# Optimization experiments

Measured on AMD Instinct MI355X. Metric: run time of the kernel, lower is better.

Reference implementation:

```python
import jax, jax.numpy as jnp
import numpy as np

THRESHOLD_FACTOR = 1.25

def setup_inputs() -> dict:
    key = jax.random.key(0)
    r_embed = jax.random.normal(key, (2, 4096, 2), dtype=jnp.float32)
    return {"r_embed": r_embed}

def reference(r_embed):
    # r_embed: [b, n, 2]
    # diff[b,s,t,i] = -r[b,s,i]*r[b,t,i] + r[b,s,i]   (einsum('bsi,bti->bsti', r, -r) + r.unsqueeze(2))
    diff = -r_embed[:, :, None, :] * r_embed[:, None, :, :] + r_embed[:, :, None, :]  # [b,s,t,2]
    dist_sq = jnp.sum(diff * diff, axis=-1)                                            # [b,s,t]
    phase_diff = jnp.arctan2(diff[..., 1], diff[..., 0])
    forward_bias = 0.5 * (1.0 + jnp.cos(phase_diff)) * jnp.exp(-dist_sq)
    mean_dist = jnp.mean(dist_sq, axis=(-1, -2), keepdims=True)
    n = dist_sq.shape[-1] * dist_sq.shape[-2]
    # torch.std default is unbiased (divide by n-1)
    var = jnp.sum((dist_sq - mean_dist) ** 2, axis=(-1, -2), keepdims=True) / (n - 1)
    std_dist = jnp.maximum(jnp.sqrt(var), 1e-6)
    threshold = mean_dist + THRESHOLD_FACTOR * std_dist
    valid_mask = (dist_sq <= threshold).astype(dist_sq.dtype)
    attention = valid_mask * forward_bias
    row_sums = jnp.sum(attention, axis=-1, keepdims=True)
    attention = attention / (row_sums + 1e-8)
    return attention
```

## Files before the change

### kernel.cpp

```cpp
#include <hip/hip_runtime.h>
#include <math.h>

#define N 4096
#define NB 2
#define THRESHOLD_FACTOR 1.25

__global__ __launch_bounds__(256) void stats_kernel(const float* __restrict__ r,
                                                    float* __restrict__ thr) {
    int b = blockIdx.x;
    const float* rb = r + (size_t)b * N * 2;
    int tid = threadIdx.x;

    double s[10];
#pragma unroll
    for (int i = 0; i < 10; ++i) s[i] = 0.0;

    for (int idx = tid; idx < N; idx += 256) {
        float x = rb[idx * 2 + 0];
        float y = rb[idx * 2 + 1];
        double a  = (double)x * (double)x;
        double bb = (double)y * (double)y;
        double ax = 1.0 - (double)x;
        double by = 1.0 - (double)y;
        double A  = ax * ax;
        double Bv = by * by;
        s[0] += a;      s[1] += bb;      s[2] += A;      s[3] += Bv;
        s[4] += a * a;  s[5] += bb * bb; s[6] += a * bb;
        s[7] += A * A;  s[8] += Bv * Bv; s[9] += A * Bv;
    }

    __shared__ double red[256][10];
#pragma unroll
    for (int q = 0; q < 10; ++q) red[tid][q] = s[q];
    __syncthreads();
    for (int st = 128; st > 0; st >>= 1) {
        if (tid < st) {
#pragma unroll
            for (int q = 0; q < 10; ++q) red[tid][q] += red[tid + st][q];
        }
        __syncthreads();
    }

    if (tid == 0) {
        double t0 = red[0][0], t1 = red[0][1], t2 = red[0][2], t3 = red[0][3];
        double t4 = red[0][4], t5 = red[0][5], t6 = red[0][6];
        double t7 = red[0][7], t8 = red[0][8], t9 = red[0][9];
        double pairs = (double)N * (double)N;
        double sum_d  = t0 * t2 + t1 * t3;
        double sum_d2 = t4 * t7 + t5 * t8 + 2.0 * t6 * t9;
        double mean = sum_d / pairs;
        double var = (sum_d2 - sum_d * sum_d / pairs) / (pairs - 1.0);
        double sd = sqrt(var);
        if (sd < 1e-6) sd = 1e-6;
        thr[b] = (float)(mean + THRESHOLD_FACTOR * sd);
    }
}

__global__ __launch_bounds__(256) void attn_kernel(const float* __restrict__ r,
                                                   const float* __restrict__ thr,
                                                   float* __restrict__ out) {
    int row = blockIdx.x;
    int b = row >> 12;
    int s = row & (N - 1);
    const float* rb = r + (size_t)b * N * 2;

    float rsx = rb[s * 2 + 0];
    float rsy = rb[s * 2 + 1];
    float threshold = thr[b];

    int tid = threadIdx.x;
    float vals[16];
    float sum = 0.0f;

#pragma unroll
    for (int g = 0; g < 4; ++g) {
        int t0 = g * 1024 + tid * 4;
        float4 p0 = *(const float4*)(rb + (size_t)t0 * 2);
        float4 p1 = *(const float4*)(rb + (size_t)t0 * 2 + 4);
        float tx[4] = {p0.x, p0.z, p1.x, p1.z};
        float ty[4] = {p0.y, p0.w, p1.y, p1.w};
#pragma unroll
        for (int k = 0; k < 4; ++k) {
            float dx = fmaf(-rsx, tx[k], rsx);
            float dy = fmaf(-rsy, ty[k], rsy);
            float d = fmaf(dx, dx, dy * dy);
            float c = (d > 0.0f) ? (dx * __builtin_amdgcn_rsqf(d)) : 1.0f;
            float e = __expf(-d);
            float fb = fmaf(0.5f, c * e, 0.5f * e);
            float v = (d <= threshold) ? fb : 0.0f;
            vals[g * 4 + k] = v;
            sum += v;
        }
    }

#pragma unroll
    for (int off = 32; off > 0; off >>= 1) sum += __shfl_down(sum, off, 64);
    __shared__ float wsum[4];
    int lane = tid & 63;
    int wid = tid >> 6;
    if (lane == 0) wsum[wid] = sum;
    __syncthreads();
    float total = wsum[0] + wsum[1] + wsum[2] + wsum[3];
    float inv = __builtin_amdgcn_rcpf(total + 1e-8f);

    float4* outp = (float4*)(out + (size_t)row * N);
#pragma unroll
    for (int g = 0; g < 4; ++g) {
        int t0 = g * 1024 + tid * 4;
        float4 v4;
        v4.x = vals[g * 4 + 0] * inv;
        v4.y = vals[g * 4 + 1] * inv;
        v4.z = vals[g * 4 + 2] * inv;
        v4.w = vals[g * 4 + 3] * inv;
        outp[t0 >> 2] = v4;
    }
}

extern "C" void kernel_launch(void* const* d_in, const int* in_sizes, int n_in,
                              void* d_out, int out_size, void* d_ws, size_t ws_size,
                              hipStream_t stream) {
    const float* r = (const float*)d_in[0];
    float* out = (float*)d_out;
    float* thr = (float*)d_ws;

    stats_kernel<<<NB, 256, 0, stream>>>(r, thr);
    attn_kernel<<<NB * N, 256, 0, stream>>>(r, thr, out);
}
```

Baseline: 143.9 us.

## Use nontemporal output stores, hoist loads, and shuffle-reduce stats with 1024 threads

The attention kernel now writes its output rows with nontemporal stores, so the 134 MB write stream bypasses normal cache retention. All eight float4 neighbour loads are issued before any compute, and one multiply is folded into an FMA. The stats kernel moves from 256 to 1024 threads and replaces its shared-memory tree reduction with wavefront shuffles plus a small cross-wave sum. These changes mainly target the write-bandwidth-bound main kernel and the serial tail of the stats kernel.

```diff
diff --git a/kernel.cpp b/kernel.cpp
--- a/kernel.cpp
+++ b/kernel.cpp
@@ -5,8 +5,10 @@
 #define NB 2
 #define THRESHOLD_FACTOR 1.25
 
-__global__ __launch_bounds__(256) void stats_kernel(const float* __restrict__ r,
-                                                    float* __restrict__ thr) {
+typedef float v4f __attribute__((ext_vector_type(4)));
+
+__global__ __launch_bounds__(1024) void stats_kernel(const float* __restrict__ r,
+                                                     float* __restrict__ thr) {
     int b = blockIdx.x;
     const float* rb = r + (size_t)b * N * 2;
     int tid = threadIdx.x;
@@ -15,7 +17,9 @@
 #pragma unroll
     for (int i = 0; i < 10; ++i) s[i] = 0.0;
 
-    for (int idx = tid; idx < N; idx += 256) {
+#pragma unroll
+    for (int it = 0; it < N / 1024; ++it) {
+        int idx = it * 1024 + tid;
         float x = rb[idx * 2 + 0];
         float y = rb[idx * 2 + 1];
         double a  = (double)x * (double)x;
@@ -29,25 +33,33 @@
         s[7] += A * A;  s[8] += Bv * Bv; s[9] += A * Bv;
     }
 
-    __shared__ double red[256][10];
 #pragma unroll
-    for (int q = 0; q < 10; ++q) red[tid][q] = s[q];
-    __syncthreads();
-    for (int st = 128; st > 0; st >>= 1) {
-        if (tid < st) {
+    for (int q = 0; q < 10; ++q) {
 #pragma unroll
-            for (int q = 0; q < 10; ++q) red[tid][q] += red[tid + st][q];
-        }
-        __syncthreads();
+        for (int off = 32; off > 0; off >>= 1) s[q] += __shfl_down(s[q], off, 64);
     }
 
+    __shared__ double wsums[16][10];
+    __shared__ double tot[10];
+    int lane = tid & 63;
+    int wid = tid >> 6;
+    if (lane == 0) {
+#pragma unroll
+        for (int q = 0; q < 10; ++q) wsums[wid][q] = s[q];
+    }
+    __syncthreads();
+    if (tid < 10) {
+        double acc = 0.0;
+#pragma unroll
+        for (int w = 0; w < 16; ++w) acc += wsums[w][tid];
+        tot[tid] = acc;
+    }
+    __syncthreads();
+
     if (tid == 0) {
-        double t0 = red[0][0], t1 = red[0][1], t2 = red[0][2], t3 = red[0][3];
-        double t4 = red[0][4], t5 = red[0][5], t6 = red[0][6];
-        double t7 = red[0][7], t8 = red[0][8], t9 = red[0][9];
         double pairs = (double)N * (double)N;
-        double sum_d  = t0 * t2 + t1 * t3;
-        double sum_d2 = t4 * t7 + t5 * t8 + 2.0 * t6 * t9;
+        double sum_d  = tot[0] * tot[2] + tot[1] * tot[3];
+        double sum_d2 = tot[4] * tot[7] + tot[5] * tot[8] + 2.0 * tot[6] * tot[9];
         double mean = sum_d / pairs;
         double var = (sum_d2 - sum_d * sum_d / pairs) / (pairs - 1.0);
         double sd = sqrt(var);
@@ -69,24 +81,29 @@
     float threshold = thr[b];
 
     int tid = threadIdx.x;
-    float vals[16];
-    float sum = 0.0f;
 
+    float4 p[4][2];
 #pragma unroll
     for (int g = 0; g < 4; ++g) {
         int t0 = g * 1024 + tid * 4;
-        float4 p0 = *(const float4*)(rb + (size_t)t0 * 2);
-        float4 p1 = *(const float4*)(rb + (size_t)t0 * 2 + 4);
-        float tx[4] = {p0.x, p0.z, p1.x, p1.z};
-        float ty[4] = {p0.y, p0.w, p1.y, p1.w};
+        p[g][0] = *(const float4*)(rb + (size_t)t0 * 2);
+        p[g][1] = *(const float4*)(rb + (size_t)t0 * 2 + 4);
+    }
+
+    float vals[16];
+    float sum = 0.0f;
+#pragma unroll
+    for (int g = 0; g < 4; ++g) {
+        float tx[4] = {p[g][0].x, p[g][0].z, p[g][1].x, p[g][1].z};
+        float ty[4] = {p[g][0].y, p[g][0].w, p[g][1].y, p[g][1].w};
 #pragma unroll
         for (int k = 0; k < 4; ++k) {
             float dx = fmaf(-rsx, tx[k], rsx);
             float dy = fmaf(-rsy, ty[k], rsy);
             float d = fmaf(dx, dx, dy * dy);
             float c = (d > 0.0f) ? (dx * __builtin_amdgcn_rsqf(d)) : 1.0f;
-            float e = __expf(-d);
-            float fb = fmaf(0.5f, c * e, 0.5f * e);
+            float h = 0.5f * __expf(-d);
+            float fb = fmaf(c, h, h);
             float v = (d <= threshold) ? fb : 0.0f;
             vals[g * 4 + k] = v;
             sum += v;
@@ -103,16 +120,16 @@
     float total = wsum[0] + wsum[1] + wsum[2] + wsum[3];
     float inv = __builtin_amdgcn_rcpf(total + 1e-8f);
 
-    float4* outp = (float4*)(out + (size_t)row * N);
+    v4f* outp = (v4f*)(out + (size_t)row * N);
 #pragma unroll
     for (int g = 0; g < 4; ++g) {
         int t0 = g * 1024 + tid * 4;
-        float4 v4;
+        v4f v4;
         v4.x = vals[g * 4 + 0] * inv;
         v4.y = vals[g * 4 + 1] * inv;
         v4.z = vals[g * 4 + 2] * inv;
         v4.w = vals[g * 4 + 3] * inv;
-        outp[t0 >> 2] = v4;
+        __builtin_nontemporal_store(v4, &outp[t0 >> 2]);
     }
 }
 
@@ -123,6 +140,6 @@
     float* out = (float*)d_out;
     float* thr = (float*)d_ws;
 
-    stats_kernel<<<NB, 256, 0, stream>>>(r, thr);
+    stats_kernel<<<NB, 1024, 0, stream>>>(r, thr);
     attn_kernel<<<NB * N, 256, 0, stream>>>(r, thr, out);
 }
```

Result: no change. 145.1 us (+0.9%).
